# Optimization experiments

Hardware: AMD Instinct MI355X
Metric: run time of the kernel (lower is better)

Reference implementation:

```python
import jax, jax.numpy as jnp
import numpy as np

B, N, NS, C, H = 2, 2048, 2048, 512, 8
HD = C // H
SCALE = HD ** -0.5
NEG = -10000.0


def setup_inputs() -> dict:
    key = jax.random.key(0)
    ks = jax.random.split(key, 9)
    q = jax.random.normal(ks[0], (B, N, C), dtype=jnp.float32)
    k = jax.random.normal(ks[1], (B, NS, C), dtype=jnp.float32)
    v = jax.random.normal(ks[2], (B, NS, C), dtype=jnp.float32)
    # 1.0 marks invalid support positions (gets -10000 added)
    supp_valid_mask = (jax.random.uniform(ks[3], (B, NS)) < 0.2).astype(jnp.float32)
    # binary fg/bg support mask used for cycle consistency
    supp_mask = jax.random.randint(ks[4], (B, NS), 0, 2, dtype=jnp.int32)
    w = 0.02
    Wq = jax.random.normal(ks[5], (C, C), dtype=jnp.float32) * w
    Wk = jax.random.normal(ks[6], (C, C), dtype=jnp.float32) * w
    Wv = jax.random.normal(ks[7], (C, C), dtype=jnp.float32) * w
    Wproj = jax.random.normal(ks[8], (C, C), dtype=jnp.float32) * w
    return {"q": q, "k": k, "v": v, "supp_valid_mask": supp_valid_mask,
            "supp_mask": supp_mask, "Wq": Wq, "Wk": Wk, "Wv": Wv, "Wproj": Wproj}


def reference(q, k, v, supp_valid_mask, supp_mask, Wq, Wk, Wv, Wproj):
    b, n, c = q.shape
    ns = k.shape[1]
    # linear projections (torch Linear: x @ W^T), split heads -> [B,H,N,HD]
    qh = (q @ Wq.T).reshape(b, n, H, HD).transpose(0, 2, 1, 3)
    kh = (k @ Wk.T).reshape(b, ns, H, HD).transpose(0, 2, 1, 3)
    vh = (v @ Wv.T).reshape(b, ns, H, HD).transpose(0, 2, 1, 3)
    attn = jnp.einsum('bhnd,bhmd->bhnm', qh, kh) * SCALE  # [B,H,N,NS]

    # cycle-consistency association (vectorized over heads)
    k2q = jnp.argmax(attn, axis=2)                    # [B,H,NS] idx into N
    q2k = jnp.argmax(attn, axis=3)                    # [B,H,N]  idx into NS
    re_map_idx = jnp.take_along_axis(q2k, k2q, axis=2)  # [B,H,NS]
    sm = jnp.broadcast_to(supp_mask[:, None, :], (b, H, ns))
    re_map_mask = jnp.take_along_axis(sm, re_map_idx, axis=2)
    asso = sm == re_map_mask                          # [B,H,NS] bool

    # mark cycle-inconsistent positions invalid (eval: ass_drop is identity)
    valid = jnp.broadcast_to(supp_valid_mask[:, None, :], (b, H, ns))
    valid = jnp.where(asso, valid, 1.0)

    attn = attn + (valid * NEG)[:, :, None, :]
    attn = jax.nn.softmax(attn, axis=-1)
    x = jnp.einsum('bhnm,bhmd->bhnd', attn, vh)       # [B,H,N,HD]
    x = x.transpose(0, 2, 1, 3).reshape(b, n, c)
    return x @ Wproj.T
```

## Files before the change

kernel.cpp:

```cpp
#include <hip/hip_runtime.h>
#include <hip/hip_bf16.h>
#include <stdint.h>

#define H_ 8
#define NS_ 2048
#define C_ 512
#define HD_ 64
#define SCALE_ 0.125f
#define NEG_ -10000.0f
#define LOG2E_ 1.4426950408889634f
#define MFIX_ 4.0f

typedef _Float16 f16x8_t __attribute__((ext_vector_type(8)));
typedef _Float16 f16x4_t __attribute__((ext_vector_type(4)));
typedef __fp16 h16x2_t __attribute__((ext_vector_type(2)));
typedef float f32x4_t __attribute__((ext_vector_type(4)));

#define MFMAH(a, b, c) __builtin_amdgcn_mfma_f32_16x16x32_f16(a, b, c, 0, 0, 0)

__device__ inline f16x8_t load_h8(const _Float16* p) {
    return *reinterpret_cast<const f16x8_t*>(p);
}

__device__ inline void gload_lds16(const void* g, void* l) {
    __builtin_amdgcn_global_load_lds(
        (const __attribute__((address_space(1))) unsigned int*)g,
        (__attribute__((address_space(3))) unsigned int*)l, 16, 0, 0);
}

__device__ inline unsigned orderF(float v) {
    unsigned u = __float_as_uint(v);
    return (u & 0x80000000u) ? ~u : (u | 0x80000000u);
}
__device__ inline unsigned long long packVR(float v, int idx) {
    return ((unsigned long long)orderF(v) << 32) | (unsigned)(~idx);
}
__device__ inline unsigned long long max64(unsigned long long a, unsigned long long b) {
    return a > b ? a : b;
}
__device__ inline unsigned long long shflx64(unsigned long long x, int m) {
    unsigned lo = (unsigned)x, hi = (unsigned)(x >> 32);
    lo = __shfl_xor(lo, m, 64);
    hi = __shfl_xor(hi, m, 64);
    return ((unsigned long long)hi << 32) | lo;
}

__global__ __launch_bounds__(256) void wsplit4(
        const float* __restrict__ w0, const float* __restrict__ w1,
        const float* __restrict__ w2, const float* __restrict__ w3,
        _Float16* __restrict__ hi, _Float16* __restrict__ lo)
{
    const int i = blockIdx.x * 256 + threadIdx.x;
    const int y = blockIdx.y;
    const float* src = (y == 0) ? w0 : (y == 1) ? w1 : (y == 2) ? w2 : w3;
    const float4 v = reinterpret_cast<const float4*>(src)[i];
    f16x4_t hv, lv;
    hv[0] = (_Float16)v.x; hv[1] = (_Float16)v.y;
    hv[2] = (_Float16)v.z; hv[3] = (_Float16)v.w;
    lv[0] = (_Float16)(v.x - (float)hv[0]);
    lv[1] = (_Float16)(v.y - (float)hv[1]);
    lv[2] = (_Float16)(v.z - (float)hv[2]);
    lv[3] = (_Float16)(v.w - (float)hv[3]);
    const size_t o = ((size_t)y << 16) + i;
    reinterpret_cast<f16x4_t*>(hi)[o] = hv;
    reinterpret_cast<f16x4_t*>(lo)[o] = lv;
}

__global__ __launch_bounds__(256) void proj_gemm(
        const float* __restrict__ qin, const float* __restrict__ kin,
        const float* __restrict__ vin,
        const _Float16* __restrict__ wHall, const _Float16* __restrict__ wLall,
        _Float16* __restrict__ qhi, _Float16* __restrict__ qlo,
        _Float16* __restrict__ khi, _Float16* __restrict__ klo,
        _Float16* __restrict__ vT)
{
    __shared__ __attribute__((aligned(16))) _Float16 Wsh[2][2][4096];
    const int zz = blockIdx.z;
    const float* A32 = (zz == 0) ? qin : (zz == 1) ? kin : vin;
    const _Float16* Wh = wHall + ((size_t)zz << 18);
    const _Float16* Wl = wLall + ((size_t)zz << 18);
    const int t = threadIdx.x, w = t >> 6, lane = t & 63;
    const int m16 = lane & 15, quad = lane >> 4;
    const int bm = blockIdx.x << 7, bn = blockIdx.y << 6;
    const int r0 = bm + (w << 5) + m16, r1 = r0 + 16;
    const int krow = lane >> 3, kblk = (lane & 7) ^ (krow & 7);
    const int e = m16 & 7;
    const int s00 = (quad ^ e) << 3, s01 = ((4 + quad) ^ e) << 3;
    const f32x4_t z = {0.f, 0.f, 0.f, 0.f};
    f32x4_t acc[2][4];
    #pragma unroll
    for (int rs = 0; rs < 2; rs++)
        #pragma unroll
        for (int tl = 0; tl < 4; tl++) acc[rs][tl] = z;

    auto stageW = [&](int buf, int kc) {
        #pragma unroll
        for (int ci = 0; ci < 4; ci++) {
            const int pp = (w << 2) + ci;
            const int s = pp >> 3, pj = pp & 7;
            const _Float16* src = (s ? Wl : Wh)
                + (size_t)(bn + (pj << 3) + krow) * C_ + kc + (kblk << 3);
            gload_lds16(src, &Wsh[buf][s][pj << 9]);
        }
    };
    auto loadA = [&](int kc, f16x8_t* d) {
        #pragma unroll
        for (int rs = 0; rs < 2; rs++) {
            const float* pr = A32 + (size_t)(rs ? r1 : r0) * C_ + kc + (quad << 3);
            #pragma unroll
            for (int seg = 0; seg < 2; seg++) {
                f16x8_t hv, lv;
                #pragma unroll
                for (int i = 0; i < 8; i++) {
                    const float x = pr[seg * 32 + i];
                    const _Float16 hh = (_Float16)x;
                    hv[i] = hh;
                    lv[i] = (_Float16)(x - (float)hh);
                }
                d[rs * 4 + seg] = hv;
                d[rs * 4 + seg + 2] = lv;
            }
        }
    };

    f16x8_t cA[8], nA[8];
    stageW(0, 0);
    loadA(0, cA);
    for (int ch = 0; ch < 8; ch++) {
        __syncthreads();
        if (ch + 1 < 8) {
            stageW((ch + 1) & 1, (ch + 1) << 6);
            loadA((ch + 1) << 6, nA);
        }
        const _Float16* W0 = Wsh[ch & 1][0];
        const _Float16* W1 = Wsh[ch & 1][1];
        #pragma unroll
        for (int tl = 0; tl < 4; tl++) {
            const int j64 = ((tl << 4) + m16) << 6;
            const f16x8_t bh0 = load_h8(&W0[j64 + s00]);
            const f16x8_t bh1 = load_h8(&W0[j64 + s01]);
            const f16x8_t bl0 = load_h8(&W1[j64 + s00]);
            const f16x8_t bl1 = load_h8(&W1[j64 + s01]);
            f32x4_t c0 = acc[0][tl];
            c0 = MFMAH(cA[0], bh0, c0); c0 = MFMAH(cA[1], bh1, c0);
            c0 = MFMAH(cA[2], bh0, c0); c0 = MFMAH(cA[3], bh1, c0);
            c0 = MFMAH(cA[0], bl0, c0); c0 = MFMAH(cA[1], bl1, c0);
            acc[0][tl] = c0;
            f32x4_t c1 = acc[1][tl];
            c1 = MFMAH(cA[4], bh0, c1); c1 = MFMAH(cA[5], bh1, c1);
            c1 = MFMAH(cA[6], bh0, c1); c1 = MFMAH(cA[7], bh1, c1);
            c1 = MFMAH(cA[4], bl0, c1); c1 = MFMAH(cA[5], bl1, c1);
            acc[1][tl] = c1;
        }
        #pragma unroll
        for (int i = 0; i < 8; i++) cA[i] = nA[i];
    }
    const int by = blockIdx.y;
    _Float16* o1 = (zz == 0) ? qhi : khi;
    _Float16* o2 = (zz == 0) ? qlo : klo;
    #pragma unroll
    for (int rs = 0; rs < 2; rs++) {
        #pragma unroll
        for (int tl = 0; tl < 4; tl++) {
            #pragma unroll
            for (int r = 0; r < 4; r++) {
                const int gr = bm + (w << 5) + (rs << 4) + (quad << 2) + r;
                const float val = acc[rs][tl][r];
                const int b = gr >> 11, n = gr & 2047;
                const int d = (tl << 4) + m16;
                const int bh = (b << 3) + by;
                if (zz == 2) {
                    const int kp = (((n >> 2) & 3) << 3) | (((n >> 4) & 1) << 2) | (n & 3);
                    vT[(((size_t)((bh << 6) + (n >> 5)) << 6) + d) * 32 + kp] = (_Float16)val;
                } else {
                    const size_t idx = ((((size_t)bh << 11) + n) << 6) + d;
                    const _Float16 hh = (_Float16)val;
                    o1[idx] = hh;
                    o2[idx] = (_Float16)(val - (float)hh);
                }
            }
        }
    }
}

__global__ __launch_bounds__(256) void argmax_mfma(
        const _Float16* __restrict__ qhi, const _Float16* __restrict__ qlo,
        const _Float16* __restrict__ khi, const _Float16* __restrict__ klo,
        unsigned long long* __restrict__ rowP, unsigned long long* __restrict__ colP)
{
    __shared__ __attribute__((aligned(16))) _Float16 Ksh[2][2][4096];
    __shared__ unsigned long long colbest[512];
    const int bx = blockIdx.x;
    const int bh = ((bx & 7) << 1) | (bx >> 9);
    const int mid = (bx >> 3) & 63;
    const int rt = mid & 15;
    const int ks = mid >> 4;
    const int t = threadIdx.x, w = t >> 6, lane = t & 63;
    const int m16 = lane & 15, quad = lane >> 4;
    const int wrow = (rt << 7) + (w << 5);
    const size_t qoff0 = ((((size_t)bh << 11) + wrow + m16) << 6) + (quad << 3);
    const size_t qoff1 = qoff0 + 1024;
    const f16x8_t a00h = load_h8(qhi + qoff0), a01h = load_h8(qhi + qoff0 + 32);
    const f16x8_t a00l = load_h8(qlo + qoff0), a01l = load_h8(qlo + qoff0 + 32);
    const f16x8_t a10h = load_h8(qhi + qoff1), a11h = load_h8(qhi + qoff1 + 32);
    const f16x8_t a10l = load_h8(qlo + qoff1), a11l = load_h8(qlo + qoff1 + 32);
    for (int c = t; c < 512; c += 256) colbest[c] = 0;
    const int krow = lane >> 3, kblk = (lane & 7) ^ (krow & 7);
    const int e = m16 & 7;
    const int s00 = (quad ^ e) << 3, s01 = ((4 + quad) ^ e) << 3;
    const size_t kbase = (((size_t)bh << 11) + (ks << 9)) << 6;
    float bv0[4] = {-3.4e38f, -3.4e38f, -3.4e38f, -3.4e38f};
    float bv1[4] = {-3.4e38f, -3.4e38f, -3.4e38f, -3.4e38f};
    int bc0[4] = {0, 0, 0, 0}, bc1[4] = {0, 0, 0, 0};
    const f32x4_t z = {0.f, 0.f, 0.f, 0.f};

    auto stage = [&](int buf, int cidx) {
        const size_t ce = kbase + ((size_t)cidx << 12);
        #pragma unroll
        for (int ci = 0; ci < 4; ci++) {
            const int pp = (w << 2) + ci;
            const int s = pp >> 3, pj = pp & 7;
            const _Float16* src = (s ? klo : khi) + ce + (((pj << 3) + krow) << 6) + (kblk << 3);
            gload_lds16(src, &Ksh[buf][s][pj << 9]);
        }
    };

    stage(0, 0);
    for (int ch = 0; ch < 8; ch++) {
        __syncthreads();
        if (ch + 1 < 8) stage((ch + 1) & 1, ch + 1);
        const _Float16* K0 = Ksh[ch & 1][0];
        const _Float16* K1 = Ksh[ch & 1][1];
        const int kc0 = (ks << 9) + (ch << 6);
        #pragma unroll
        for (int tl = 0; tl < 4; tl++) {
            const int j64 = ((tl << 4) + m16) << 6;
            const f16x8_t bh0 = load_h8(&K0[j64 + s00]);
            const f16x8_t bh1 = load_h8(&K0[j64 + s01]);
            const f16x8_t bl0 = load_h8(&K1[j64 + s00]);
            const f16x8_t bl1 = load_h8(&K1[j64 + s01]);
            f32x4_t c0 = MFMAH(a00h, bh0, z);
            c0 = MFMAH(a01h, bh1, c0);
            c0 = MFMAH(a00l, bh0, c0); c0 = MFMAH(a01l, bh1, c0);
            c0 = MFMAH(a00h, bl0, c0); c0 = MFMAH(a01h, bl1, c0);
            f32x4_t c1 = MFMAH(a10h, bh0, z);
            c1 = MFMAH(a11h, bh1, c1);
            c1 = MFMAH(a10l, bh0, c1); c1 = MFMAH(a11l, bh1, c1);
            c1 = MFMAH(a10h, bl0, c1); c1 = MFMAH(a11h, bl1, c1);
            const int gc = kc0 + (tl << 4) + m16;
            #pragma unroll
            for (int r = 0; r < 4; r++) {
                if (c0[r] > bv0[r]) { bv0[r] = c0[r]; bc0[r] = gc; }
                if (c1[r] > bv1[r]) { bv1[r] = c1[r]; bc1[r] = gc; }
            }
            float v = c0[0]; int ri = (quad << 2);
            if (c0[1] > v) { v = c0[1]; ri = (quad << 2) + 1; }
            if (c0[2] > v) { v = c0[2]; ri = (quad << 2) + 2; }
            if (c0[3] > v) { v = c0[3]; ri = (quad << 2) + 3; }
            if (c1[0] > v) { v = c1[0]; ri = 16 + (quad << 2); }
            if (c1[1] > v) { v = c1[1]; ri = 16 + (quad << 2) + 1; }
            if (c1[2] > v) { v = c1[2]; ri = 16 + (quad << 2) + 2; }
            if (c1[3] > v) { v = c1[3]; ri = 16 + (quad << 2) + 3; }
            unsigned long long pk = packVR(v, wrow + ri);
            pk = max64(pk, shflx64(pk, 16));
            pk = max64(pk, shflx64(pk, 32));
            if (quad == 0) atomicMax(&colbest[(ch << 6) + (tl << 4) + m16], pk);
        }
    }
    #pragma unroll
    for (int r = 0; r < 4; r++) {
        unsigned long long p0 = packVR(bv0[r], bc0[r]);
        p0 = max64(p0, shflx64(p0, 1)); p0 = max64(p0, shflx64(p0, 2));
        p0 = max64(p0, shflx64(p0, 4)); p0 = max64(p0, shflx64(p0, 8));
        if (m16 == 0)
            atomicMax(rowP + ((size_t)bh << 11) + wrow + (quad << 2) + r, p0);
        unsigned long long p1 = packVR(bv1[r], bc1[r]);
        p1 = max64(p1, shflx64(p1, 1)); p1 = max64(p1, shflx64(p1, 2));
        p1 = max64(p1, shflx64(p1, 4)); p1 = max64(p1, shflx64(p1, 8));
        if (m16 == 0)
            atomicMax(rowP + ((size_t)bh << 11) + wrow + 16 + (quad << 2) + r, p1);
    }
    __syncthreads();
    for (int c = t; c < 512; c += 256)
        atomicMax(colP + ((size_t)bh << 11) + (ks << 9) + c, colbest[c]);
}

__global__ __launch_bounds__(256) void resolve(const unsigned long long* __restrict__ q2kP,
        const unsigned long long* __restrict__ k2qP, const int* __restrict__ supp_mask,
        const float* __restrict__ supp_valid, float* __restrict__ vn)
{
    const int t = blockIdx.x * 256 + threadIdx.x;
    const int bh = t >> 11, j = t & 2047, b = bh >> 3;
    const unsigned k2q = 0xFFFFFFFFu - (unsigned)(k2qP[t] & 0xFFFFFFFFull);
    const unsigned rm  = 0xFFFFFFFFu - (unsigned)(q2kP[(bh << 11) + k2q] & 0xFFFFFFFFull);
    const int asso = supp_mask[(b << 11) + j] == supp_mask[(b << 11) + (int)rm];
    const float valid = asso ? supp_valid[(b << 11) + j] : 1.0f;
    vn[t] = fmaf(valid, NEG_ * LOG2E_, -MFIX_);
}

__global__ __launch_bounds__(256) void attn_pv(
        const _Float16* __restrict__ qh, const _Float16* __restrict__ kh,
        const _Float16* __restrict__ vT, const float* __restrict__ vnG,
        float* __restrict__ xp, float* __restrict__ lp)
{
    __shared__ __attribute__((aligned(16))) _Float16 Ksh[2][2048];
    __shared__ __attribute__((aligned(16))) _Float16 Vsh[2][2048];
    __shared__ __attribute__((aligned(16))) float vnL[1024];
    const int bx = blockIdx.x;
    const int bh = ((bx & 7) << 1) | (bx >> 9);
    const int mid = (bx >> 3) & 63;
    const int rt = mid & 31, ks = mid >> 5;
    const int t = threadIdx.x, w = t >> 6, lane = t & 63;
    const int m16 = lane & 15, quad = lane >> 4;
    const int rowbase = (rt << 6) + (w << 4);
    const size_t qoff = ((((size_t)bh << 11) + rowbase + m16) << 6) + (quad << 3);
    const f16x8_t a0 = load_h8(qh + qoff), a1 = load_h8(qh + qoff + 32);
    for (int c = t; c < 1024; c += 256) vnL[c] = vnG[(bh << 11) + (ks << 10) + c];
    const float KS = SCALE_ * LOG2E_;
    const int krow = lane >> 3, kblk = (lane & 7) ^ ((lane >> 3) & 7);
    const int vrow = lane >> 2, vblk = (lane & 3) ^ ((lane >> 3) & 3);
    const int e = m16 & 7;
    const int s00 = (quad ^ e) << 3, s01 = ((4 + quad) ^ e) << 3;
    const int vsw = (m16 >> 1) & 3;
    f16x8_t ones;
    #pragma unroll
    for (int i = 0; i < 8; i++) ones[i] = (_Float16)1.0f;
    const f32x4_t z = {0.f, 0.f, 0.f, 0.f};
    f32x4_t xacc[4];
    #pragma unroll
    for (int nt = 0; nt < 4; nt++) xacc[nt] = z;
    f32x4_t lacc = z;

    const size_t kbel = ((size_t)bh << 11) * HD_;
    const bool isK = (w < 2);
    const _Float16* src0;
    const _Float16* src1;
    _Float16* dst0a; _Float16* dst0b; _Float16* dst1a; _Float16* dst1b;
    if (isK) {
        const int call0 = w << 1;
        src0 = kh + kbel + ((size_t)ks << 16) + (((call0 << 3) + krow) << 6) + (kblk << 3);
        src1 = src0 + 512;
        dst0a = &Ksh[0][call0 << 9]; dst0b = &Ksh[1][call0 << 9];
        dst1a = &Ksh[0][(call0 + 1) << 9]; dst1b = &Ksh[1][(call0 + 1) << 9];
    } else {
        const int j0 = (w - 2) << 1;
        src0 = vT + (((size_t)(bh << 6) + (ks << 5)) << 11)
                  + (((j0 << 4) + vrow) << 5) + (vblk << 3);
        src1 = src0 + 512;
        dst0a = &Vsh[0][j0 << 9]; dst0b = &Vsh[1][j0 << 9];
        dst1a = &Vsh[0][(j0 + 1) << 9]; dst1b = &Vsh[1][(j0 + 1) << 9];
    }
    auto stage = [&](int buf) {
        gload_lds16(src0, buf ? dst0b : dst0a);
        gload_lds16(src1, buf ? dst1b : dst1a);
        src0 += 2048; src1 += 2048;
    };

    stage(0);
    for (int ch = 0; ch < 32; ch++) {
        __syncthreads();
        if (ch + 1 < 32) stage((ch + 1) & 1);
        const _Float16* K = Ksh[ch & 1];
        const _Float16* V = Vsh[ch & 1];
        const f16x8_t b00 = load_h8(&K[(m16 << 6) + s00]);
        const f16x8_t b01 = load_h8(&K[(m16 << 6) + s01]);
        const f16x8_t b10 = load_h8(&K[((16 + m16) << 6) + s00]);
        const f16x8_t b11 = load_h8(&K[((16 + m16) << 6) + s01]);
        f32x4_t c0 = MFMAH(b00, a0, z); c0 = MFMAH(b01, a1, c0);
        f32x4_t c1 = MFMAH(b10, a0, z); c1 = MFMAH(b11, a1, c1);
        const f32x4_t vn0 = *reinterpret_cast<const f32x4_t*>(&vnL[(ch << 5) + (quad << 2)]);
        const f32x4_t vn1 = *reinterpret_cast<const f32x4_t*>(&vnL[(ch << 5) + 16 + (quad << 2)]);
        union { h16x2_t h2[4]; f16x8_t v8; } pk;
        pk.h2[0] = __builtin_amdgcn_cvt_pkrtz(
            __builtin_amdgcn_exp2f(fmaf(c0[0], KS, vn0[0])),
            __builtin_amdgcn_exp2f(fmaf(c0[1], KS, vn0[1])));
        pk.h2[1] = __builtin_amdgcn_cvt_pkrtz(
            __builtin_amdgcn_exp2f(fmaf(c0[2], KS, vn0[2])),
            __builtin_amdgcn_exp2f(fmaf(c0[3], KS, vn0[3])));
        pk.h2[2] = __builtin_amdgcn_cvt_pkrtz(
            __builtin_amdgcn_exp2f(fmaf(c1[0], KS, vn1[0])),
            __builtin_amdgcn_exp2f(fmaf(c1[1], KS, vn1[1])));
        pk.h2[3] = __builtin_amdgcn_cvt_pkrtz(
            __builtin_amdgcn_exp2f(fmaf(c1[2], KS, vn1[2])),
            __builtin_amdgcn_exp2f(fmaf(c1[3], KS, vn1[3])));
        const f16x8_t pa = pk.v8;
        lacc = MFMAH(pa, ones, lacc);
        #pragma unroll
        for (int nt = 0; nt < 4; nt++) {
            const f16x8_t vb = load_h8(&V[((nt * 16 + m16) << 5) + ((quad ^ vsw) << 3)]);
            xacc[nt] = MFMAH(pa, vb, xacc[nt]);
        }
    }
    const int b = bh >> 3, h = bh & 7;
    if (m16 == 0) {
        #pragma unroll
        for (int r = 0; r < 4; r++)
            lp[((size_t)ks << 15) + (bh << 11) + rowbase + (quad << 2) + r] = lacc[r];
    }
    const size_t xbase = ((size_t)ks << 21);
    #pragma unroll
    for (int r = 0; r < 4; r++) {
        const int row = rowbase + (quad << 2) + r;
        #pragma unroll
        for (int nt = 0; nt < 4; nt++)
            xp[xbase + (((size_t)(b << 11) + row) << 9) + (h << 6) + (nt << 4) + m16] = xacc[nt][r];
    }
}

__global__ __launch_bounds__(256) void out_gemm(
        const float* __restrict__ xp, const float* __restrict__ lp,
        const _Float16* __restrict__ Wh, const _Float16* __restrict__ Wl,
        float* __restrict__ outF)
{
    __shared__ __attribute__((aligned(16))) _Float16 Wsh[2][2][4096];
    const int t = threadIdx.x, w = t >> 6, lane = t & 63;
    const int m16 = lane & 15, quad = lane >> 4;
    const int bm = blockIdx.x << 7, bn = blockIdx.y << 6;
    const int r0 = bm + (w << 5) + m16, r1 = r0 + 16;
    const int krow = lane >> 3, kblk = (lane & 7) ^ (krow & 7);
    const int e = m16 & 7;
    const int s00 = (quad ^ e) << 3, s01 = ((4 + quad) ^ e) << 3;
    const f32x4_t z = {0.f, 0.f, 0.f, 0.f};
    f32x4_t acc[2][4];
    #pragma unroll
    for (int rs = 0; rs < 2; rs++)
        #pragma unroll
        for (int tl = 0; tl < 4; tl++) acc[rs][tl] = z;

    auto stageW = [&](int buf, int kc) {
        #pragma unroll
        for (int ci = 0; ci < 4; ci++) {
            const int pp = (w << 2) + ci;
            const int s = pp >> 3, pj = pp & 7;
            const _Float16* src = (s ? Wl : Wh)
                + (size_t)(bn + (pj << 3) + krow) * C_ + kc + (kblk << 3);
            gload_lds16(src, &Wsh[buf][s][pj << 9]);
        }
    };
    auto loadA = [&](int ch, f16x8_t* d) {
        const int kc = ch << 6;
        #pragma unroll
        for (int rs = 0; rs < 2; rs++) {
            const int r = rs ? r1 : r0;
            const int b = r >> 11, n = r & 2047;
            const size_t li = ((size_t)((b << 3) + ch) << 11) + n;
            const float linv = 1.0f / (lp[li] + lp[32768 + li]);
            const size_t base = ((size_t)r << 9) + kc + (quad << 3);
            #pragma unroll
            for (int seg = 0; seg < 2; seg++) {
                f16x8_t hv, lv;
                #pragma unroll
                for (int i = 0; i < 8; i++) {
                    const size_t o = base + seg * 32 + i;
                    const float x = (xp[o] + xp[2097152 + o]) * linv;
                    const _Float16 hh = (_Float16)x;
                    hv[i] = hh;
                    lv[i] = (_Float16)(x - (float)hh);
                }
                d[rs * 4 + seg] = hv;
                d[rs * 4 + seg + 2] = lv;
            }
        }
    };

    f16x8_t cA[8], nA[8];
    stageW(0, 0);
    loadA(0, cA);
    for (int ch = 0; ch < 8; ch++) {
        __syncthreads();
        if (ch + 1 < 8) {
            stageW((ch + 1) & 1, (ch + 1) << 6);
            loadA(ch + 1, nA);
        }
        const _Float16* W0 = Wsh[ch & 1][0];
        const _Float16* W1 = Wsh[ch & 1][1];
        #pragma unroll
        for (int tl = 0; tl < 4; tl++) {
            const int j64 = ((tl << 4) + m16) << 6;
            const f16x8_t bh0 = load_h8(&W0[j64 + s00]);
            const f16x8_t bh1 = load_h8(&W0[j64 + s01]);
            const f16x8_t bl0 = load_h8(&W1[j64 + s00]);
            const f16x8_t bl1 = load_h8(&W1[j64 + s01]);
            f32x4_t c0 = acc[0][tl];
            c0 = MFMAH(cA[0], bh0, c0); c0 = MFMAH(cA[1], bh1, c0);
            c0 = MFMAH(cA[2], bh0, c0); c0 = MFMAH(cA[3], bh1, c0);
            c0 = MFMAH(cA[0], bl0, c0); c0 = MFMAH(cA[1], bl1, c0);
            acc[0][tl] = c0;
            f32x4_t c1 = acc[1][tl];
            c1 = MFMAH(cA[4], bh0, c1); c1 = MFMAH(cA[5], bh1, c1);
            c1 = MFMAH(cA[6], bh0, c1); c1 = MFMAH(cA[7], bh1, c1);
            c1 = MFMAH(cA[4], bl0, c1); c1 = MFMAH(cA[5], bl1, c1);
            acc[1][tl] = c1;
        }
        #pragma unroll
        for (int i = 0; i < 8; i++) cA[i] = nA[i];
    }
    #pragma unroll
    for (int rs = 0; rs < 2; rs++) {
        #pragma unroll
        for (int tl = 0; tl < 4; tl++) {
            #pragma unroll
            for (int r = 0; r < 4; r++) {
                const int gr = bm + (w << 5) + (rs << 4) + (quad << 2) + r;
                const int gj = bn + (tl << 4) + m16;
                outF[(size_t)gr * C_ + gj] = acc[rs][tl][r];
            }
        }
    }
}

extern "C" void kernel_launch(void* const* d_in, const int* in_sizes, int n_in,
                              void* d_out, int out_size, void* d_ws, size_t ws_size,
                              hipStream_t stream) {
    const float* q  = (const float*)d_in[0];
    const float* k  = (const float*)d_in[1];
    const float* v  = (const float*)d_in[2];
    const float* supp_valid = (const float*)d_in[3];
    const int*   supp_mask  = (const int*)d_in[4];
    const float* Wq = (const float*)d_in[5];
    const float* Wk = (const float*)d_in[6];
    const float* Wv = (const float*)d_in[7];
    const float* Wp = (const float*)d_in[8];
    float* out = (float*)d_out;

    char* p = (char*)d_ws;
    _Float16* qhi = (_Float16*)p;      p += 4194304;
    _Float16* qlo = (_Float16*)p;      p += 4194304;
    _Float16* khi = (_Float16*)p;      p += 4194304;
    _Float16* klo = (_Float16*)p;      p += 4194304;
    _Float16* vT  = (_Float16*)p;      p += 4194304;
    float* xp     = (float*)p;         p += 16777216;
    _Float16* wH  = (_Float16*)p;      p += 2097152;
    _Float16* wL  = (_Float16*)p;      p += 2097152;
    unsigned long long* q2kP = (unsigned long long*)p; p += 262144;
    unsigned long long* k2qP = (unsigned long long*)p; p += 262144;
    float* lp = (float*)p;             p += 262144;
    float* validNeg = (float*)p;       p += 131072;

    (void)hipMemsetAsync(q2kP, 0, 524288, stream);

    dim3 bG(256);
    wsplit4<<<dim3(256, 4), bG, 0, stream>>>(Wq, Wk, Wv, Wp, wH, wL);
    proj_gemm<<<dim3(32, 8, 3), bG, 0, stream>>>(q, k, v, wH, wL,
                                                 qhi, qlo, khi, klo, vT);

    argmax_mfma<<<1024, bG, 0, stream>>>(qhi, qlo, khi, klo, q2kP, k2qP);

    resolve<<<128, bG, 0, stream>>>(q2kP, k2qP, supp_mask, supp_valid, validNeg);

    attn_pv<<<1024, bG, 0, stream>>>(qhi, khi, vT, validNeg, xp, lp);

    out_gemm<<<dim3(32, 8), bG, 0, stream>>>(xp, lp,
                                             wH + 3 * 262144, wL + 3 * 262144, out);
}
```

Measured before the change: 214.8 us.

## Double rows per wave in attn_pv and deepen K/V LDS pipeline to four buffers

Each wave of attn_pv now handles 32 query rows instead of 16, so every K/V tile staged in LDS is reused across twice as many rows, and the grid shrinks from 1024 to 512 blocks. The K/V staging ring grows from two to four buffers with a prefetch distance of two, and explicit vmcnt waits plus a raw s_barrier replace the per-iteration __syncthreads. This cuts LDS and global traffic per unit of work and hides load latency better. In exchange it uses more registers and LDS per block and leaves fewer blocks to fill the GPU.

New measurement: 209.2 us. 1.03x faster.

```diff
diff --git a/kernel.cpp b/kernel.cpp
--- a/kernel.cpp
+++ b/kernel.cpp
@@ -303,18 +303,19 @@
         const _Float16* __restrict__ vT, const float* __restrict__ vnG,
         float* __restrict__ xp, float* __restrict__ lp)
 {
-    __shared__ __attribute__((aligned(16))) _Float16 Ksh[2][2048];
-    __shared__ __attribute__((aligned(16))) _Float16 Vsh[2][2048];
+    __shared__ __attribute__((aligned(16))) _Float16 Ksh[4][2048];
+    __shared__ __attribute__((aligned(16))) _Float16 Vsh[4][2048];
     __shared__ __attribute__((aligned(16))) float vnL[1024];
     const int bx = blockIdx.x;
-    const int bh = ((bx & 7) << 1) | (bx >> 9);
-    const int mid = (bx >> 3) & 63;
-    const int rt = mid & 31, ks = mid >> 5;
+    const int bh = ((bx & 7) << 1) | (bx >> 8);
+    const int mid = (bx >> 3) & 31;
+    const int rt = mid & 15, ks = mid >> 4;
     const int t = threadIdx.x, w = t >> 6, lane = t & 63;
     const int m16 = lane & 15, quad = lane >> 4;
-    const int rowbase = (rt << 6) + (w << 4);
+    const int rowbase = (rt << 7) + (w << 5);
     const size_t qoff = ((((size_t)bh << 11) + rowbase + m16) << 6) + (quad << 3);
     const f16x8_t a0 = load_h8(qh + qoff), a1 = load_h8(qh + qoff + 32);
+    const f16x8_t a2 = load_h8(qh + qoff + 1024), a3 = load_h8(qh + qoff + 1056);
     for (int c = t; c < 1024; c += 256) vnL[c] = vnG[(bh << 11) + (ks << 10) + c];
     const float KS = SCALE_ * LOG2E_;
     const int krow = lane >> 3, kblk = (lane & 7) ^ ((lane >> 3) & 7);
@@ -326,84 +327,112 @@
     #pragma unroll
     for (int i = 0; i < 8; i++) ones[i] = (_Float16)1.0f;
     const f32x4_t z = {0.f, 0.f, 0.f, 0.f};
-    f32x4_t xacc[4];
-    #pragma unroll
-    for (int nt = 0; nt < 4; nt++) xacc[nt] = z;
-    f32x4_t lacc = z;
+    f32x4_t xacc0[4], xacc1[4];
+    #pragma unroll
+    for (int nt = 0; nt < 4; nt++) { xacc0[nt] = z; xacc1[nt] = z; }
+    f32x4_t lacc0 = z, lacc1 = z;
 
     const size_t kbel = ((size_t)bh << 11) * HD_;
     const bool isK = (w < 2);
     const _Float16* src0;
     const _Float16* src1;
-    _Float16* dst0a; _Float16* dst0b; _Float16* dst1a; _Float16* dst1b;
+    _Float16* dstA;
+    _Float16* dstB;
     if (isK) {
         const int call0 = w << 1;
         src0 = kh + kbel + ((size_t)ks << 16) + (((call0 << 3) + krow) << 6) + (kblk << 3);
         src1 = src0 + 512;
-        dst0a = &Ksh[0][call0 << 9]; dst0b = &Ksh[1][call0 << 9];
-        dst1a = &Ksh[0][(call0 + 1) << 9]; dst1b = &Ksh[1][(call0 + 1) << 9];
+        dstA = &Ksh[0][call0 << 9];
+        dstB = &Ksh[0][(call0 + 1) << 9];
     } else {
         const int j0 = (w - 2) << 1;
         src0 = vT + (((size_t)(bh << 6) + (ks << 5)) << 11)
                   + (((j0 << 4) + vrow) << 5) + (vblk << 3);
         src1 = src0 + 512;
-        dst0a = &Vsh[0][j0 << 9]; dst0b = &Vsh[1][j0 << 9];
-        dst1a = &Vsh[0][(j0 + 1) << 9]; dst1b = &Vsh[1][(j0 + 1) << 9];
-    }
-    auto stage = [&](int buf) {
-        gload_lds16(src0, buf ? dst0b : dst0a);
-        gload_lds16(src1, buf ? dst1b : dst1a);
+        dstA = &Vsh[0][j0 << 9];
+        dstB = &Vsh[0][(j0 + 1) << 9];
+    }
+    auto stage = [&](int bufidx) {
+        gload_lds16(src0, dstA + (bufidx << 11));
+        gload_lds16(src1, dstB + (bufidx << 11));
         src0 += 2048; src1 += 2048;
     };
 
+    __syncthreads();
     stage(0);
+    stage(1);
     for (int ch = 0; ch < 32; ch++) {
-        __syncthreads();
-        if (ch + 1 < 32) stage((ch + 1) & 1);
-        const _Float16* K = Ksh[ch & 1];
-        const _Float16* V = Vsh[ch & 1];
+        if (ch < 31) { asm volatile("s_waitcnt vmcnt(2)" ::: "memory"); }
+        else         { asm volatile("s_waitcnt vmcnt(0)" ::: "memory"); }
+        __builtin_amdgcn_sched_barrier(0);
+        __builtin_amdgcn_s_barrier();
+        __builtin_amdgcn_sched_barrier(0);
+        if (ch + 2 < 32) stage((ch + 2) & 3);
+        const _Float16* K = Ksh[ch & 3];
+        const _Float16* V = Vsh[ch & 3];
         const f16x8_t b00 = load_h8(&K[(m16 << 6) + s00]);
         const f16x8_t b01 = load_h8(&K[(m16 << 6) + s01]);
         const f16x8_t b10 = load_h8(&K[((16 + m16) << 6) + s00]);
         const f16x8_t b11 = load_h8(&K[((16 + m16) << 6) + s01]);
         f32x4_t c0 = MFMAH(b00, a0, z); c0 = MFMAH(b01, a1, c0);
         f32x4_t c1 = MFMAH(b10, a0, z); c1 = MFMAH(b11, a1, c1);
+        f32x4_t c2 = MFMAH(b00, a2, z); c2 = MFMAH(b01, a3, c2);
+        f32x4_t c3 = MFMAH(b10, a2, z); c3 = MFMAH(b11, a3, c3);
         const f32x4_t vn0 = *reinterpret_cast<const f32x4_t*>(&vnL[(ch << 5) + (quad << 2)]);
         const f32x4_t vn1 = *reinterpret_cast<const f32x4_t*>(&vnL[(ch << 5) + 16 + (quad << 2)]);
-        union { h16x2_t h2[4]; f16x8_t v8; } pk;
-        pk.h2[0] = __builtin_amdgcn_cvt_pkrtz(
+        union { h16x2_t h2[4]; f16x8_t v8; } pk0, pk1;
+        pk0.h2[0] = __builtin_amdgcn_cvt_pkrtz(
             __builtin_amdgcn_exp2f(fmaf(c0[0], KS, vn0[0])),
             __builtin_amdgcn_exp2f(fmaf(c0[1], KS, vn0[1])));
-        pk.h2[1] = __builtin_amdgcn_cvt_pkrtz(
+        pk0.h2[1] = __builtin_amdgcn_cvt_pkrtz(
             __builtin_amdgcn_exp2f(fmaf(c0[2], KS, vn0[2])),
             __builtin_amdgcn_exp2f(fmaf(c0[3], KS, vn0[3])));
-        pk.h2[2] = __builtin_amdgcn_cvt_pkrtz(
+        pk0.h2[2] = __builtin_amdgcn_cvt_pkrtz(
             __builtin_amdgcn_exp2f(fmaf(c1[0], KS, vn1[0])),
             __builtin_amdgcn_exp2f(fmaf(c1[1], KS, vn1[1])));
-        pk.h2[3] = __builtin_amdgcn_cvt_pkrtz(
+        pk0.h2[3] = __builtin_amdgcn_cvt_pkrtz(
             __builtin_amdgcn_exp2f(fmaf(c1[2], KS, vn1[2])),
             __builtin_amdgcn_exp2f(fmaf(c1[3], KS, vn1[3])));
-        const f16x8_t pa = pk.v8;
-        lacc = MFMAH(pa, ones, lacc);
+        pk1.h2[0] = __builtin_amdgcn_cvt_pkrtz(
+            __builtin_amdgcn_exp2f(fmaf(c2[0], KS, vn0[0])),
+            __builtin_amdgcn_exp2f(fmaf(c2[1], KS, vn0[1])));
+        pk1.h2[1] = __builtin_amdgcn_cvt_pkrtz(
+            __builtin_amdgcn_exp2f(fmaf(c2[2], KS, vn0[2])),
+            __builtin_amdgcn_exp2f(fmaf(c2[3], KS, vn0[3])));
+        pk1.h2[2] = __builtin_amdgcn_cvt_pkrtz(
+            __builtin_amdgcn_exp2f(fmaf(c3[0], KS, vn1[0])),
+            __builtin_amdgcn_exp2f(fmaf(c3[1], KS, vn1[1])));
+        pk1.h2[3] = __builtin_amdgcn_cvt_pkrtz(
+            __builtin_amdgcn_exp2f(fmaf(c3[2], KS, vn1[2])),
+            __builtin_amdgcn_exp2f(fmaf(c3[3], KS, vn1[3])));
+        const f16x8_t pa0 = pk0.v8, pa1 = pk1.v8;
+        lacc0 = MFMAH(pa0, ones, lacc0);
+        lacc1 = MFMAH(pa1, ones, lacc1);
         #pragma unroll
         for (int nt = 0; nt < 4; nt++) {
             const f16x8_t vb = load_h8(&V[((nt * 16 + m16) << 5) + ((quad ^ vsw) << 3)]);
-            xacc[nt] = MFMAH(pa, vb, xacc[nt]);
+            xacc0[nt] = MFMAH(pa0, vb, xacc0[nt]);
+            xacc1[nt] = MFMAH(pa1, vb, xacc1[nt]);
         }
     }
     const int b = bh >> 3, h = bh & 7;
     if (m16 == 0) {
         #pragma unroll
-        for (int r = 0; r < 4; r++)
-            lp[((size_t)ks << 15) + (bh << 11) + rowbase + (quad << 2) + r] = lacc[r];
+        for (int r = 0; r < 4; r++) {
+            lp[((size_t)ks << 15) + (bh << 11) + rowbase + (quad << 2) + r] = lacc0[r];
+            lp[((size_t)ks << 15) + (bh << 11) + rowbase + 16 + (quad << 2) + r] = lacc1[r];
+        }
     }
     const size_t xbase = ((size_t)ks << 21);
     #pragma unroll
     for (int r = 0; r < 4; r++) {
-        const int row = rowbase + (quad << 2) + r;
-        #pragma unroll
-        for (int nt = 0; nt < 4; nt++)
-            xp[xbase + (((size_t)(b << 11) + row) << 9) + (h << 6) + (nt << 4) + m16] = xacc[nt][r];
+        const int row0 = rowbase + (quad << 2) + r;
+        const int row1 = row0 + 16;
+        #pragma unroll
+        for (int nt = 0; nt < 4; nt++) {
+            xp[xbase + (((size_t)(b << 11) + row0) << 9) + (h << 6) + (nt << 4) + m16] = xacc0[nt][r];
+            xp[xbase + (((size_t)(b << 11) + row1) << 9) + (h << 6) + (nt << 4) + m16] = xacc1[nt][r];
+        }
     }
 }
 
@@ -548,7 +577,7 @@
 
     resolve<<<128, bG, 0, stream>>>(q2kP, k2qP, supp_mask, supp_valid, validNeg);
 
-    attn_pv<<<1024, bG, 0, stream>>>(qhi, khi, vT, validNeg, xp, lp);
+    attn_pv<<<512, bG, 0, stream>>>(qhi, khi, vT, validNeg, xp, lp);
 
     out_gemm<<<dim3(32, 8), bG, 0, stream>>>(xp, lp,
                                              wH + 3 * 262144, wL + 3 * 262144, out);
```
